# Kernel tuning notes

Hardware: AMD Instinct MI355X
Metric: run time of the kernel (lower is better)

## Reference

```python
import jax, jax.numpy as jnp
import numpy as np

WINDOW_SIZE = 11
CHANNEL = 1
SIGMA = 1.5


def _gaussian_window(window_size=WINDOW_SIZE, channel=CHANNEL, sigma=SIGMA):
    x = np.arange(window_size)
    g = np.exp(-((x - window_size // 2) ** 2) / (2.0 * sigma ** 2))
    g = g / g.sum()
    w2d = np.outer(g, g).astype(np.float32)  # [K,K]
    # depthwise conv kernel: [C_out=channel, C_in/groups=1, K, K]
    return jnp.asarray(np.broadcast_to(w2d, (channel, 1, window_size, window_size)))


def _dwconv(x, window):
    pad = WINDOW_SIZE // 2
    return jax.lax.conv_general_dilated(
        x, window,
        window_strides=(1, 1),
        padding=[(pad, pad), (pad, pad)],
        dimension_numbers=('NCHW', 'OIHW', 'NCHW'),
        feature_group_count=CHANNEL)


def _ssim(img1, img2, window):
    C1 = 0.01 ** 2
    C2 = 0.03 ** 2
    mu1 = _dwconv(img1, window)
    mu2 = _dwconv(img2, window)
    mu1_sq = mu1 * mu1
    mu2_sq = mu2 * mu2
    mu1_mu2 = mu1 * mu2
    sigma1_sq = _dwconv(img1 * img1, window) - mu1_sq
    sigma2_sq = _dwconv(img2 * img2, window) - mu2_sq
    sigma12 = _dwconv(img1 * img2, window) - mu1_mu2
    ssim_map = ((2.0 * mu1_mu2 + C1) * (2.0 * sigma12 + C2)) / (
        (mu1_sq + mu2_sq + C1) * (sigma1_sq + sigma2_sq + C2))
    return ssim_map.mean()


def setup_inputs() -> dict:
    key = jax.random.key(0)
    k1, k2 = jax.random.split(key)
    B, C, H, W = 64, 1, 512, 512
    pred = jax.random.uniform(k1, (B, C, H, W), dtype=jnp.float32)
    target = jax.random.uniform(k2, (B, C, H, W), dtype=jnp.float32)
    return {"pred": pred, "target": target}


def reference(pred, target):
    window = _gaussian_window()
    return 1.0 - _ssim(pred[:, :1], target[:, :1], window)
```

## Files before the change

kernel.cpp:

```cpp
#include <hip/hip_runtime.h>

#define BATCH 64
#define HH 512
#define WW 512
#define TH 32
#define KS 11
#define PADK 5
#define NIN (TH + 2 * PADK)
#define NF4 262
#define NPIX (64.0 * 512.0 * 512.0)

__global__ void __launch_bounds__(512, 2) ssim_main_kernel(
    const float* __restrict__ img1, const float* __restrict__ img2,
    double* __restrict__ accum) {
  constexpr float GA[KS] = {
      0.00102838f, 0.00759884f, 0.03600087f, 0.10936069f, 0.21300553f,
      0.26601172f, 0.21300553f, 0.10936069f, 0.03600087f, 0.00759884f,
      0.00102838f};
  const float C1v = 1e-4f, C2v = 9e-4f;

  const int t  = threadIdx.x;
  const int r0 = blockIdx.x * TH;
  const int b  = blockIdx.y;

  const float2* __restrict__ pp1 =
      reinterpret_cast<const float2*>(img1 + (size_t)b * HH * WW);
  const float2* __restrict__ pp2 =
      reinterpret_cast<const float2*>(img2 + (size_t)b * HH * WW);

  __shared__ float4 s4[2][4][NF4];
  __shared__ float wsum[8];

  if (t < 6) {
    const int idx = (t < 3) ? t : (256 + t);
#pragma unroll
    for (int bi = 0; bi < 2; ++bi)
#pragma unroll
      for (int r = 0; r < 4; ++r) s4[bi][r][idx] = make_float4(0.f, 0.f, 0.f, 0.f);
  }

  const int pi = t & 255;
  const int jA = (t >> 8) & 1;
  const int jB = jA + 2;
  const int base = pi + jA;

#define RFL(x) __int_as_float(__builtin_amdgcn_readfirstlane(__float_as_int(x)))
  const bool oddp = ((__builtin_amdgcn_readfirstlane(t) >> 8) & 1) != 0;
  const float wx0 = RFL(oddp ? GA[0]  : 0.f);
  const float wx1 = RFL(oddp ? GA[2]  : GA[1]);
  const float wx2 = RFL(oddp ? GA[4]  : GA[3]);
  const float wx3 = RFL(oddp ? GA[6]  : GA[5]);
  const float wx4 = RFL(oddp ? GA[8]  : GA[7]);
  const float wx5 = RFL(oddp ? GA[10] : GA[9]);
  const float wz0 = RFL(oddp ? GA[1]  : GA[0]);
  const float wz1 = RFL(oddp ? GA[3]  : GA[2]);
  const float wz2 = RFL(oddp ? GA[5]  : GA[4]);
  const float wz3 = RFL(oddp ? GA[7]  : GA[6]);
  const float wz4 = RFL(oddp ? GA[9]  : GA[8]);
  const float wz5 = RFL(oddp ? 0.f    : GA[10]);

#define DECLR(s) float zA##s = 0.f, zB##s = 0.f, zQ##s = 0.f, zP##s = 0.f;
  DECLR(0) DECLR(1) DECLR(2) DECLR(3) DECLR(4) DECLR(5)
  DECLR(6) DECLR(7) DECLR(8) DECLR(9) DECLR(10)

  float2 taA, tbA, taB, tbB;
  float local = 0.f;

#define LOADC(k_) {                                                     \
    taA = make_float2(0.f, 0.f); tbA = make_float2(0.f, 0.f);           \
    taB = make_float2(0.f, 0.f); tbB = make_float2(0.f, 0.f);           \
    { const int rr_ = r0 - PADK + 4 * (k_) + jA;                        \
      if ((unsigned)rr_ < HH) { const int o_ = rr_ * (WW / 2) + pi;     \
        taA = pp1[o_]; tbA = pp2[o_]; } }                               \
    if (4 * (k_) + jB < NIN) {                                          \
      const int rr_ = r0 - PADK + 4 * (k_) + jB;                        \
      if ((unsigned)rr_ < HH) { const int o_ = rr_ * (WW / 2) + pi;     \
        taB = pp1[o_]; tbB = pp2[o_]; } } }

#define WRITEC(k_) {                                                    \
    s4[(k_) & 1][jA][pi + 3] = make_float4(taA.x, tbA.x, taA.y, tbA.y); \
    if (4 * (k_) + jB < NIN)                                            \
      s4[(k_) & 1][jB][pi + 3] =                                        \
          make_float4(taB.x, tbB.x, taB.y, tbB.y); }

#define HK(bb_, j_, kk_, wx_, wz_) {                                    \
    const float4 v = s4[bb_][j_][base + kk_];                           \
    const float qx_ = fmaf(v.x, v.x, v.y * v.y);                        \
    const float px_ = v.x * v.y;                                        \
    h1 = fmaf(wx_, v.x, h1); h2 = fmaf(wx_, v.y, h2);                   \
    hq = fmaf(wx_, qx_, hq); hp = fmaf(wx_, px_, hp);                   \
    const float qz_ = fmaf(v.z, v.z, v.w * v.w);                        \
    const float pz_ = v.z * v.w;                                        \
    h1 = fmaf(wz_, v.z, h1); h2 = fmaf(wz_, v.w, h2);                   \
    hq = fmaf(wz_, qz_, hq); hp = fmaf(wz_, pz_, hp); }

#define HBODY(bb_, j_, S) {                                             \
    float h1 = 0.f, h2 = 0.f, hq = 0.f, hp = 0.f;                       \
    HK(bb_, j_, 0, wx0, wz0) HK(bb_, j_, 1, wx1, wz1)                   \
    HK(bb_, j_, 2, wx2, wz2) HK(bb_, j_, 3, wx3, wz3)                   \
    HK(bb_, j_, 4, wx4, wz4) HK(bb_, j_, 5, wx5, wz5)                   \
    zA##S = h1; zB##S = h2; zQ##S = hq; zP##S = hp; }

#define VC(P, s0,s1,s2v,s3,s4v,s5,s6v,s7,s8,s9,s10)                     \
  fmaf(GA[10], P##s10, fmaf(GA[9], P##s9, fmaf(GA[8], P##s8,            \
  fmaf(GA[7], P##s7, fmaf(GA[6], P##s6v, fmaf(GA[5], P##s5,             \
  fmaf(GA[4], P##s4v, fmaf(GA[3], P##s3, fmaf(GA[2], P##s2v,            \
  fmaf(GA[1], P##s1, GA[0] * P##s0))))))))))

#define VOUTBODY(s0,s1,s2v,s3,s4v,s5,s6v,s7,s8,s9,s10)                  \
  {                                                                     \
    const float m1 = VC(zA, s0,s1,s2v,s3,s4v,s5,s6v,s7,s8,s9,s10);      \
    const float m2 = VC(zB, s0,s1,s2v,s3,s4v,s5,s6v,s7,s8,s9,s10);      \
    const float mq = VC(zQ, s0,s1,s2v,s3,s4v,s5,s6v,s7,s8,s9,s10);      \
    const float mp = VC(zP, s0,s1,s2v,s3,s4v,s5,s6v,s7,s8,s9,s10);      \
    const float m1s = m1 * m1, m2s = m2 * m2, m12 = m1 * m2;            \
    const float s12 = mp - m12;                                         \
    const float sqq = mq - m1s - m2s;                                   \
    const float num = fmaf(2.f, m12, C1v) * fmaf(2.f, s12, C2v);        \
    const float den = (m1s + m2s + C1v) * (sqq + C2v);                  \
    local = fmaf(num, __builtin_amdgcn_rcpf(den), local);               \
  }

#define ROT0  0,1,2,3,4,5,6,7,8,9,10
#define ROT1  1,2,3,4,5,6,7,8,9,10,0
#define ROT2  2,3,4,5,6,7,8,9,10,0,1
#define ROT3  3,4,5,6,7,8,9,10,0,1,2
#define ROT4  4,5,6,7,8,9,10,0,1,2,3
#define ROT5  5,6,7,8,9,10,0,1,2,3,4
#define ROT6  6,7,8,9,10,0,1,2,3,4,5
#define ROT7  7,8,9,10,0,1,2,3,4,5,6
#define ROT8  8,9,10,0,1,2,3,4,5,6,7
#define ROT9  9,10,0,1,2,3,4,5,6,7,8
#define ROT10 10,0,1,2,3,4,5,6,7,8,9
#define VOUTE(...) VOUTBODY(__VA_ARGS__)

#define ROWH(bb_, j_, S)      { HBODY(bb_, j_, S) }
#define ROWO(bb_, j_, S, R_)  { HBODY(bb_, j_, S) VOUTE(R_) }

  LOADC(0)

  WRITEC(0) __syncthreads(); LOADC(1)
  ROWH(0,0,0) ROWH(0,1,1) ROWH(0,2,2) ROWH(0,3,3)
  WRITEC(1) __syncthreads(); LOADC(2)
  ROWH(1,0,4) ROWH(1,1,5) ROWH(1,2,6) ROWH(1,3,7)
  WRITEC(2) __syncthreads(); LOADC(3)
  ROWH(0,0,8) ROWH(0,1,9)
  ROWO(0,2,10, ROT0) ROWO(0,3,0, ROT1)
  WRITEC(3) __syncthreads(); LOADC(4)
  ROWO(1,0,1, ROT2) ROWO(1,1,2, ROT3) ROWO(1,2,3, ROT4) ROWO(1,3,4, ROT5)
  WRITEC(4) __syncthreads(); LOADC(5)
  ROWO(0,0,5, ROT6) ROWO(0,1,6, ROT7) ROWO(0,2,7, ROT8) ROWO(0,3,8, ROT9)
  WRITEC(5) __syncthreads(); LOADC(6)
  ROWO(1,0,9, ROT10) ROWO(1,1,10, ROT0) ROWO(1,2,0, ROT1) ROWO(1,3,1, ROT2)
  WRITEC(6) __syncthreads(); LOADC(7)
  ROWO(0,0,2, ROT3) ROWO(0,1,3, ROT4) ROWO(0,2,4, ROT5) ROWO(0,3,5, ROT6)
  WRITEC(7) __syncthreads(); LOADC(8)
  ROWO(1,0,6, ROT7) ROWO(1,1,7, ROT8) ROWO(1,2,8, ROT9) ROWO(1,3,9, ROT10)
  WRITEC(8) __syncthreads(); LOADC(9)
  ROWO(0,0,10, ROT0) ROWO(0,1,0, ROT1) ROWO(0,2,1, ROT2) ROWO(0,3,2, ROT3)
  WRITEC(9) __syncthreads(); LOADC(10)
  ROWO(1,0,3, ROT4) ROWO(1,1,4, ROT5) ROWO(1,2,5, ROT6) ROWO(1,3,6, ROT7)
  WRITEC(10) __syncthreads();
  ROWO(0,0,7, ROT8) ROWO(0,1,8, ROT9)

#pragma unroll
  for (int off = 32; off > 0; off >>= 1) local += __shfl_down(local, off, 64);
  const int wave = t >> 6;
  const int lane = t & 63;
  if (lane == 0) wsum[wave] = local;
  __syncthreads();
  if (t == 0) {
    float s = 0.f;
#pragma unroll
    for (int w = 0; w < 8; ++w) s += wsum[w];
    atomicAdd(accum, (double)s);
  }
}

__global__ void ssim_final_kernel(const double* __restrict__ accum,
                                  float* __restrict__ out) {
  out[0] = 1.0f - (float)(accum[0] / NPIX);
}

extern "C" void kernel_launch(void* const* d_in, const int* in_sizes, int n_in,
                              void* d_out, int out_size, void* d_ws, size_t ws_size,
                              hipStream_t stream) {
  const float* img1 = (const float*)d_in[0];
  const float* img2 = (const float*)d_in[1];
  double* accum = (double*)d_ws;
  hipMemsetAsync(accum, 0, sizeof(double), stream);

  dim3 grid(HH / TH, BATCH);
  ssim_main_kernel<<<grid, 512, 0, stream>>>(img1, img2, accum);
  ssim_final_kernel<<<1, 1, 0, stream>>>(accum, (float*)d_out);
}
```

Before: 183.3 us.

## Convolve sum/difference images with packed FP32 math to halve VALU work

Stores s=a+b and d=a-b in shared memory instead of a and b, so the four filtered quantities (mu1, mu2, E[a²+b²], E[ab]) come from filtering s, d, s² and d². Both passes then use packed two-wide FMAs (v_pk_fma_f32), and the SSIM terms are recovered algebraically. This roughly halves the scalar FMA count in the compute-bound convolution. The cost is some float rounding change from the sum/difference transform and extra recombination arithmetic per output.

Result: no change. 186.4 us (+1.7%).

```diff
diff --git a/kernel.cpp b/kernel.cpp
--- a/kernel.cpp
+++ b/kernel.cpp
@@ -10,6 +10,15 @@
 #define NF4 262
 #define NPIX (64.0 * 512.0 * 512.0)
 
+typedef float v2f __attribute__((ext_vector_type(2)));
+static __device__ __forceinline__ v2f mk2(float x, float y) {
+  v2f r; r.x = x; r.y = y; return r;
+}
+static __device__ __forceinline__ v2f pkfma(v2f a, v2f b, v2f c) {
+#pragma clang fp contract(fast)
+  return a * b + c;
+}
+
 __global__ void __launch_bounds__(512, 2) ssim_main_kernel(
     const float* __restrict__ img1, const float* __restrict__ img2,
     double* __restrict__ accum) {
@@ -23,10 +32,10 @@
   const int r0 = blockIdx.x * TH;
   const int b  = blockIdx.y;
 
-  const float2* __restrict__ pp1 =
-      reinterpret_cast<const float2*>(img1 + (size_t)b * HH * WW);
-  const float2* __restrict__ pp2 =
-      reinterpret_cast<const float2*>(img2 + (size_t)b * HH * WW);
+  const v2f* __restrict__ pp1 =
+      reinterpret_cast<const v2f*>(img1 + (size_t)b * HH * WW);
+  const v2f* __restrict__ pp2 =
+      reinterpret_cast<const v2f*>(img2 + (size_t)b * HH * WW);
 
   __shared__ float4 s4[2][4][NF4];
   __shared__ float wsum[8];
@@ -59,16 +68,16 @@
   const float wz4 = RFL(oddp ? GA[9]  : GA[8]);
   const float wz5 = RFL(oddp ? 0.f    : GA[10]);
 
-#define DECLR(s) float zA##s = 0.f, zB##s = 0.f, zQ##s = 0.f, zP##s = 0.f;
+#define DECLR(s) v2f zV##s = {0.f, 0.f}, zW##s = {0.f, 0.f};
   DECLR(0) DECLR(1) DECLR(2) DECLR(3) DECLR(4) DECLR(5)
   DECLR(6) DECLR(7) DECLR(8) DECLR(9) DECLR(10)
 
-  float2 taA, tbA, taB, tbB;
+  v2f taA, tbA, taB, tbB;
   float local = 0.f;
 
 #define LOADC(k_) {                                                     \
-    taA = make_float2(0.f, 0.f); tbA = make_float2(0.f, 0.f);           \
-    taB = make_float2(0.f, 0.f); tbB = make_float2(0.f, 0.f);           \
+    taA = mk2(0.f, 0.f); tbA = mk2(0.f, 0.f);                           \
+    taB = mk2(0.f, 0.f); tbB = mk2(0.f, 0.f);                           \
     { const int rr_ = r0 - PADK + 4 * (k_) + jA;                        \
       if ((unsigned)rr_ < HH) { const int o_ = rr_ * (WW / 2) + pi;     \
         taA = pp1[o_]; tbA = pp2[o_]; } }                               \
@@ -78,46 +87,50 @@
         taB = pp1[o_]; tbB = pp2[o_]; } } }
 
 #define WRITEC(k_) {                                                    \
-    s4[(k_) & 1][jA][pi + 3] = make_float4(taA.x, tbA.x, taA.y, tbA.y); \
-    if (4 * (k_) + jB < NIN)                                            \
+    { const v2f sp_ = taA + tbA, dp_ = taA - tbA;                       \
+      s4[(k_) & 1][jA][pi + 3] =                                        \
+          make_float4(sp_.x, dp_.x, sp_.y, dp_.y); }                    \
+    if (4 * (k_) + jB < NIN) {                                          \
+      const v2f sp_ = taB + tbB, dp_ = taB - tbB;                       \
       s4[(k_) & 1][jB][pi + 3] =                                        \
-          make_float4(taB.x, tbB.x, taB.y, tbB.y); }
+          make_float4(sp_.x, dp_.x, sp_.y, dp_.y); } }
 
 #define HK(bb_, j_, kk_, wx_, wz_) {                                    \
     const float4 v = s4[bb_][j_][base + kk_];                           \
-    const float qx_ = fmaf(v.x, v.x, v.y * v.y);                        \
-    const float px_ = v.x * v.y;                                        \
-    h1 = fmaf(wx_, v.x, h1); h2 = fmaf(wx_, v.y, h2);                   \
-    hq = fmaf(wx_, qx_, hq); hp = fmaf(wx_, px_, hp);                   \
-    const float qz_ = fmaf(v.z, v.z, v.w * v.w);                        \
-    const float pz_ = v.z * v.w;                                        \
-    h1 = fmaf(wz_, v.z, h1); h2 = fmaf(wz_, v.w, h2);                   \
-    hq = fmaf(wz_, qz_, hq); hp = fmaf(wz_, pz_, hp); }
+    const v2f lo = mk2(v.x, v.y);                                       \
+    const v2f hi = mk2(v.z, v.w);                                       \
+    hV = pkfma(mk2(wx_, wx_), lo, hV);                                  \
+    hW = pkfma(mk2(wx_, wx_), lo * lo, hW);                             \
+    hV = pkfma(mk2(wz_, wz_), hi, hV);                                  \
+    hW = pkfma(mk2(wz_, wz_), hi * hi, hW); }
 
 #define HBODY(bb_, j_, S) {                                             \
-    float h1 = 0.f, h2 = 0.f, hq = 0.f, hp = 0.f;                       \
+    v2f hV = {0.f, 0.f}, hW = {0.f, 0.f};                               \
     HK(bb_, j_, 0, wx0, wz0) HK(bb_, j_, 1, wx1, wz1)                   \
     HK(bb_, j_, 2, wx2, wz2) HK(bb_, j_, 3, wx3, wz3)                   \
     HK(bb_, j_, 4, wx4, wz4) HK(bb_, j_, 5, wx5, wz5)                   \
-    zA##S = h1; zB##S = h2; zQ##S = hq; zP##S = hp; }
-
-#define VC(P, s0,s1,s2v,s3,s4v,s5,s6v,s7,s8,s9,s10)                     \
-  fmaf(GA[10], P##s10, fmaf(GA[9], P##s9, fmaf(GA[8], P##s8,            \
-  fmaf(GA[7], P##s7, fmaf(GA[6], P##s6v, fmaf(GA[5], P##s5,             \
-  fmaf(GA[4], P##s4v, fmaf(GA[3], P##s3, fmaf(GA[2], P##s2v,            \
-  fmaf(GA[1], P##s1, GA[0] * P##s0))))))))))
+    zV##S = hV; zW##S = hW; }
+
+#define G2(i) mk2(GA[i], GA[i])
+#define VCP(P, s0,s1,s2v,s3,s4v,s5,s6v,s7,s8,s9,s10)                    \
+  pkfma(G2(10), P##s10, pkfma(G2(9), P##s9, pkfma(G2(8), P##s8,         \
+  pkfma(G2(7), P##s7, pkfma(G2(6), P##s6v, pkfma(G2(5), P##s5,          \
+  pkfma(G2(4), P##s4v, pkfma(G2(3), P##s3, pkfma(G2(2), P##s2v,         \
+  pkfma(G2(1), P##s1, G2(0) * P##s0))))))))))
 
 #define VOUTBODY(s0,s1,s2v,s3,s4v,s5,s6v,s7,s8,s9,s10)                  \
   {                                                                     \
-    const float m1 = VC(zA, s0,s1,s2v,s3,s4v,s5,s6v,s7,s8,s9,s10);      \
-    const float m2 = VC(zB, s0,s1,s2v,s3,s4v,s5,s6v,s7,s8,s9,s10);      \
-    const float mq = VC(zQ, s0,s1,s2v,s3,s4v,s5,s6v,s7,s8,s9,s10);      \
-    const float mp = VC(zP, s0,s1,s2v,s3,s4v,s5,s6v,s7,s8,s9,s10);      \
-    const float m1s = m1 * m1, m2s = m2 * m2, m12 = m1 * m2;            \
+    const v2f mV = VCP(zV, s0,s1,s2v,s3,s4v,s5,s6v,s7,s8,s9,s10);       \
+    const v2f mW = VCP(zW, s0,s1,s2v,s3,s4v,s5,s6v,s7,s8,s9,s10);       \
+    const v2f mV2 = mV * mV;                                            \
+    const float msum = 0.5f  * (mV2.x + mV2.y);                         \
+    const float m12  = 0.25f * (mV2.x - mV2.y);                         \
+    const float mq   = 0.5f  * (mW.x + mW.y);                           \
+    const float mp   = 0.25f * (mW.x - mW.y);                           \
     const float s12 = mp - m12;                                         \
-    const float sqq = mq - m1s - m2s;                                   \
+    const float sqq = mq - msum;                                        \
     const float num = fmaf(2.f, m12, C1v) * fmaf(2.f, s12, C2v);        \
-    const float den = (m1s + m2s + C1v) * (sqq + C2v);                  \
+    const float den = (msum + C1v) * (sqq + C2v);                       \
     local = fmaf(num, __builtin_amdgcn_rcpf(den), local);               \
   }
 
```
